# Kernel optimization log

Measured on AMD Instinct MI355X. Metric: run time of the kernel, lower is better.

The kernel has to match this reference:

```python
import jax, jax.numpy as jnp
import numpy as np

IN_FEATURES = 1024
OUT_FEATURES = 1024
BATCH = 32
SEQ = 1024
EPS = 1e-8


def setup_inputs() -> dict:
    key = jax.random.key(0)
    k1, k2, k3 = jax.random.split(key, 3)
    Efou = jax.random.normal(k1, (BATCH, SEQ, IN_FEATURES), dtype=jnp.float32)
    y = jax.random.normal(k2, (BATCH, IN_FEATURES), dtype=jnp.float32)
    weight = jax.random.normal(k3, (IN_FEATURES, OUT_FEATURES), dtype=jnp.float32)
    return {"Efou": Efou, "y": y, "weight": weight}


def reference(Efou, y, weight):
    # scale = 1/sqrt(in_features)
    scale = 1.0 / np.sqrt(np.float32(weight.shape[0]))
    ys = y * scale  # (b, i) == per-sample column scaling of weight
    # Demodulation norm: sum_i (scale*W[i,o]*y[b,i])^2 = (ys^2) @ (W^2)
    d = jax.lax.rsqrt(jnp.einsum('bi,io->bo', ys * ys, weight * weight) + EPS)  # (b, o)
    # Efou @ (scale*W*y*d) == ((Efou*ys) @ W) * d  -- same math, avoids (b,i,o) weight
    out = jnp.einsum('bsi,io->bso', Efou * ys[:, None, :], weight) * d[:, None, :]
    return out
```

## Files before the change

kernel.cpp:

```cpp
#include <hip/hip_runtime.h>

#define AS1 __attribute__((address_space(1)))
#define AS3 __attribute__((address_space(3)))

typedef __bf16 bf16x8 __attribute__((ext_vector_type(8)));
typedef float f32x4 __attribute__((ext_vector_type(4)));
typedef unsigned short ushort8 __attribute__((ext_vector_type(8)));

__device__ __forceinline__ unsigned short f2bf(float f) {
  union { float f; unsigned u; } v; v.f = f;
  unsigned u = v.u;
  unsigned r = (u + 0x7fffu + ((u >> 16) & 1u)) >> 16;
  return (unsigned short)r;
}

__global__ __launch_bounds__(256) void prep_kernel(const float* __restrict__ y,
                                                   const float* __restrict__ W,
                                                   float* __restrict__ partial,
                                                   unsigned short* __restrict__ WT) {
  __shared__ float ysq[32][32];
  const int o = blockIdx.x * 256 + threadIdx.x;
  const int i0 = blockIdx.y * 32;
  for (int e = threadIdx.x; e < 1024; e += 256) {
    int il = e >> 5, b = e & 31;
    float t = y[b * 1024 + i0 + il] * 0.03125f;
    ysq[il][b] = t * t;
  }
  __syncthreads();

  f32x4 acc[8] = {};
  ushort8 wb[4];
#pragma unroll
  for (int il = 0; il < 32; ++il) {
    float w = W[(size_t)(i0 + il) * 1024 + o];
    wb[il >> 3][il & 7] = f2bf(w);
    float w2 = w * w;
#pragma unroll
    for (int b4 = 0; b4 < 8; ++b4) {
      f32x4 q = *(const f32x4*)&ysq[il][b4 * 4];
#pragma unroll
      for (int k = 0; k < 4; ++k) acc[b4][k] = fmaf(q[k], w2, acc[b4][k]);
    }
  }
  unsigned short* wt = WT + (size_t)o * 1024 + i0;
#pragma unroll
  for (int q = 0; q < 4; ++q) *(ushort8*)(wt + q * 8) = wb[q];
  float* p = partial + (size_t)blockIdx.y * 32768 + o;
#pragma unroll
  for (int b4 = 0; b4 < 8; ++b4)
#pragma unroll
    for (int k = 0; k < 4; ++k) p[(b4 * 4 + k) * 1024] = acc[b4][k];
}

__global__ __launch_bounds__(256) void xconv_kernel(const float4* __restrict__ E4,
                                                    const float* __restrict__ y,
                                                    unsigned short* __restrict__ X) {
  const size_t total = (size_t)8388608;
  for (size_t g = (size_t)blockIdx.x * blockDim.x + threadIdx.x; g < total;
       g += (size_t)gridDim.x * blockDim.x) {
    float4 v = E4[g];
    size_t e = g * 4;
    int i = (int)(e & 1023);
    int b = (int)(e >> 20);
    float4 yv = *(const float4*)(y + b * 1024 + i);
    ushort4 o;
    o.x = f2bf(v.x * yv.x * 0.03125f);
    o.y = f2bf(v.y * yv.y * 0.03125f);
    o.z = f2bf(v.z * yv.z * 0.03125f);
    o.w = f2bf(v.w * yv.w * 0.03125f);
    *(ushort4*)(X + e) = o;
  }
}

#define NT 16
#define LDS_TILE 65536

#define BAR __builtin_amdgcn_s_barrier()
#define LGKM0 asm volatile("s_waitcnt lgkmcnt(0)" ::: "memory")
#define VM(n) asm volatile("s_waitcnt vmcnt(" #n ")" ::: "memory")
#define SCHB __builtin_amdgcn_sched_barrier(0)
#define PRIO(x) __builtin_amdgcn_s_setprio(x)

#define STG_A(r, t, dst)                                                     \
  __builtin_amdgcn_global_load_lds(                                          \
      (const AS1 void*)(Xs + (size_t)(r) * 64 * 2048 + (t) * 128),           \
      (AS3 void*)((dst) + (r) * 8192 + sldso), 16, 0, 0)
#define STG_B(r, t, dst)                                                     \
  __builtin_amdgcn_global_load_lds(                                          \
      (const AS1 void*)(Ws + (size_t)(r) * 64 * 2048 + (t) * 128),           \
      (AS3 void*)((dst) + 32768 + (r) * 8192 + sldso), 16, 0, 0)

#define RD_A(mh, mi, kk)                                                     \
  (*(const bf16x8*)(Ab + (wr * 128 + ((mh) * 4 + (mi)) * 16 + l15) * 128 +   \
                    ((((kk) * 64 + lhi * 16)) ^ swz_rd)))
#define RD_B(nh, ni, kk)                                                     \
  (*(const bf16x8*)(Bb + (wc * 64 + ((nh) * 2 + (ni)) * 16 + l15) * 128 +    \
                    ((((kk) * 64 + lhi * 16)) ^ swz_rd)))

#define LD_A(mh)                                                             \
  { _Pragma("unroll") for (int mi = 0; mi < 4; ++mi)                         \
      _Pragma("unroll") for (int kk = 0; kk < 2; ++kk)                       \
        a[mi][kk] = RD_A(mh, mi, kk); }
#define LD_B(nh)                                                             \
  { _Pragma("unroll") for (int ni = 0; ni < 2; ++ni)                         \
      _Pragma("unroll") for (int kk = 0; kk < 2; ++kk)                       \
        bfr[ni][kk] = RD_B(nh, ni, kk); }

#define MM(mh, nh)                                                           \
  do {                                                                       \
    _Pragma("unroll") for (int mi = 0; mi < 4; ++mi)                         \
      _Pragma("unroll") for (int ni = 0; ni < 2; ++ni)                       \
        _Pragma("unroll") for (int kk = 0; kk < 2; ++kk)                     \
          acc[(mh) * 4 + mi][(nh) * 2 + ni] =                                \
              __builtin_amdgcn_mfma_f32_16x16x32_bf16(                       \
                  a[mi][kk], bfr[ni][kk], acc[(mh) * 4 + mi][(nh) * 2 + ni], \
                  0, 0, 0);                                                  \
  } while (0)

__global__ __launch_bounds__(512, 2) void gemm8d_kernel(
    const unsigned short* __restrict__ X, const unsigned short* __restrict__ WT,
    const float* __restrict__ dpart, float* __restrict__ out) {
  extern __shared__ char lds[];
  float* dtab = (float*)(lds + 2 * LDS_TILE);

  const int tid = threadIdx.x;
  const int bid = blockIdx.x;
  const int wg = (bid & 7) * 64 + (bid >> 3);
  const int bm = wg >> 2, bn = wg & 3;
  const int m0 = bm * 256, n0 = bn * 256;
  const int b = m0 >> 10;

  const int w = tid >> 6, l = tid & 63;
  const int wr = w >> 2, wc = w & 3;
  const int l15 = l & 15, lhi = l >> 4;
  const int swz_rd = (l15 & 7) << 4;

  const int srow = tid >> 3;
  const int scb = ((tid & 7) << 4) ^ ((srow & 7) << 4);
  const char* Xs = (const char*)X + (size_t)(m0 + srow) * 2048 + scb;
  const char* Ws = (const char*)WT + (size_t)(n0 + srow) * 2048 + scb;
  const int sldso = tid * 16;

  f32x4 acc[8][4] = {};
  bf16x8 a[4][2], bfr[2][2];

  char* buf0 = lds;
  char* buf1 = lds + LDS_TILE;

  if (tid < 256) {
    const float* dp = dpart + b * 1024 + n0 + tid;
    float s = 0.f;
#pragma unroll 8
    for (int is = 0; is < 32; ++is) s += dp[(size_t)is * 32768];
    dtab[tid] = rsqrtf(s + 1e-8f);
  }
  __syncthreads();

  STG_A(0, 0, buf0); STG_A(2, 0, buf0); STG_A(1, 0, buf0); STG_A(3, 0, buf0);
  STG_B(0, 0, buf0); STG_B(1, 0, buf0); STG_B(2, 0, buf0); STG_B(3, 0, buf0);
  STG_A(0, 1, buf1); STG_A(2, 1, buf1); STG_A(1, 1, buf1); STG_A(3, 1, buf1);
  VM(4);
  BAR;

  for (int t = 0; t < NT - 2; ++t) {
    const char* Ab = lds + (t & 1) * LDS_TILE;
    const char* Bb = Ab + 32768;
    char* dB = lds + ((t + 1) & 1) * LDS_TILE;
    char* dA = lds + (t & 1) * LDS_TILE;
    const int t1 = t + 1, t2 = t + 2;
    LD_A(0); LD_B(0);
    STG_B(0, t1, dB); STG_B(1, t1, dB);
    BAR; LGKM0; SCHB; PRIO(1); MM(0, 0); PRIO(0); SCHB; BAR;
    LD_B(1);
    STG_B(2, t1, dB); STG_B(3, t1, dB);
    BAR; LGKM0; SCHB; PRIO(1); MM(0, 1); PRIO(0); SCHB; BAR;
    LD_A(1); LD_B(0);
    STG_A(0, t2, dA); STG_A(2, t2, dA);
    BAR; LGKM0; SCHB; PRIO(1); MM(1, 0); PRIO(0); SCHB; BAR;
    LD_B(1);
    STG_A(1, t2, dA); STG_A(3, t2, dA);
    BAR; LGKM0; SCHB; PRIO(1); MM(1, 1); PRIO(0); SCHB;
    VM(4);
    BAR;
  }

  {
    const int t = NT - 2;
    const char* Ab = lds + (t & 1) * LDS_TILE;
    const char* Bb = Ab + 32768;
    char* dB = lds + ((t + 1) & 1) * LDS_TILE;
    const int t1 = t + 1;
    LD_A(0); LD_B(0);
    STG_B(0, t1, dB); STG_B(1, t1, dB);
    BAR; LGKM0; SCHB; PRIO(1); MM(0, 0); PRIO(0); SCHB; BAR;
    LD_B(1);
    STG_B(2, t1, dB); STG_B(3, t1, dB);
    BAR; LGKM0; SCHB; PRIO(1); MM(0, 1); PRIO(0); SCHB; BAR;
    LD_A(1); LD_B(0);
    BAR; LGKM0; SCHB; PRIO(1); MM(1, 0); PRIO(0); SCHB; BAR;
    LD_B(1);
    BAR; LGKM0; SCHB; PRIO(1); MM(1, 1); PRIO(0); SCHB;
    VM(0);
    BAR;
  }

  {
    const char* Ab = lds + ((NT - 1) & 1) * LDS_TILE;
    const char* Bb = Ab + 32768;
    LD_A(0); LD_B(0);
    BAR; LGKM0; SCHB; PRIO(1); MM(0, 0); PRIO(0); SCHB; BAR;
    LD_B(1);
    BAR; LGKM0; SCHB; PRIO(1); MM(0, 1); PRIO(0); SCHB; BAR;
    LD_A(1); LD_B(0);
    BAR; LGKM0; SCHB; PRIO(1); MM(1, 0); PRIO(0); SCHB; BAR;
    LD_B(1);
    BAR; LGKM0; SCHB; PRIO(1); MM(1, 1); PRIO(0); SCHB;
  }

  const int lc0 = wc * 64 + l15;
  float dv[4];
#pragma unroll
  for (int nf = 0; nf < 4; ++nf) dv[nf] = dtab[lc0 + nf * 16];
#pragma unroll
  for (int mf = 0; mf < 8; ++mf) {
#pragma unroll
    for (int j = 0; j < 4; ++j) {
      const int row = m0 + wr * 128 + mf * 16 + lhi * 4 + j;
      float* orow = out + (size_t)row * 1024 + n0 + lc0;
#pragma unroll
      for (int nf = 0; nf < 4; ++nf) orow[nf * 16] = acc[mf][nf][j] * dv[nf];
    }
  }
}

extern "C" void kernel_launch(void* const* d_in, const int* in_sizes, int n_in,
                              void* d_out, int out_size, void* d_ws, size_t ws_size,
                              hipStream_t stream) {
  const float* Efou = (const float*)d_in[0];
  const float* y    = (const float*)d_in[1];
  const float* W    = (const float*)d_in[2];
  float* out = (float*)d_out;

  unsigned short* X  = (unsigned short*)d_ws;
  unsigned short* WT = X + (size_t)32768 * 1024;
  float* dpart       = (float*)(WT + (size_t)1024 * 1024);

  hipFuncSetAttribute((const void*)gemm8d_kernel,
                      hipFuncAttributeMaxDynamicSharedMemorySize, 132096);

  prep_kernel<<<dim3(4, 32), 256, 0, stream>>>(y, W, dpart, WT);
  xconv_kernel<<<2048, 256, 0, stream>>>((const float4*)Efou, y, X);
  gemm8d_kernel<<<512, 512, 132096, stream>>>(X, WT, dpart, out);
}
```

Before: 135.1 us.

## Switch GEMM to 32x32x16 MFMA and merge prep kernels into one launch

The GEMM inner loop now uses 32x32x16 bf16 MFMA with matching fragment reads and accumulator layout instead of 16x16x32. This reduces LDS fragment loads per MFMA and instruction count. The weight-prep and Efou-conversion kernels are fused into a single launch split by block index, removing one kernel launch boundary. The epilogue is rewritten for the 32x32 accumulator layout, which changes register pressure and store patterns.

After: 152.6 us. +13.0%, slower.

```diff
diff --git a/kernel.cpp b/kernel.cpp
--- a/kernel.cpp
+++ b/kernel.cpp
@@ -5,6 +5,7 @@
 
 typedef __bf16 bf16x8 __attribute__((ext_vector_type(8)));
 typedef float f32x4 __attribute__((ext_vector_type(4)));
+typedef float f32x16 __attribute__((ext_vector_type(16)));
 typedef unsigned short ushort8 __attribute__((ext_vector_type(8)));
 
 __device__ __forceinline__ unsigned short f2bf(float f) {
@@ -14,61 +15,60 @@
   return (unsigned short)r;
 }
 
-__global__ __launch_bounds__(256) void prep_kernel(const float* __restrict__ y,
-                                                   const float* __restrict__ W,
-                                                   float* __restrict__ partial,
-                                                   unsigned short* __restrict__ WT) {
+__global__ __launch_bounds__(256) void prepx_kernel(
+    const float* __restrict__ y, const float* __restrict__ W,
+    const float4* __restrict__ E4, float* __restrict__ partial,
+    unsigned short* __restrict__ WT, unsigned short* __restrict__ X) {
   __shared__ float ysq[32][32];
-  const int o = blockIdx.x * 256 + threadIdx.x;
-  const int i0 = blockIdx.y * 32;
-  for (int e = threadIdx.x; e < 1024; e += 256) {
-    int il = e >> 5, b = e & 31;
-    float t = y[b * 1024 + i0 + il] * 0.03125f;
-    ysq[il][b] = t * t;
-  }
-  __syncthreads();
-
-  f32x4 acc[8] = {};
-  ushort8 wb[4];
-#pragma unroll
-  for (int il = 0; il < 32; ++il) {
-    float w = W[(size_t)(i0 + il) * 1024 + o];
-    wb[il >> 3][il & 7] = f2bf(w);
-    float w2 = w * w;
-#pragma unroll
-    for (int b4 = 0; b4 < 8; ++b4) {
-      f32x4 q = *(const f32x4*)&ysq[il][b4 * 4];
-#pragma unroll
-      for (int k = 0; k < 4; ++k) acc[b4][k] = fmaf(q[k], w2, acc[b4][k]);
-    }
-  }
-  unsigned short* wt = WT + (size_t)o * 1024 + i0;
-#pragma unroll
-  for (int q = 0; q < 4; ++q) *(ushort8*)(wt + q * 8) = wb[q];
-  float* p = partial + (size_t)blockIdx.y * 32768 + o;
-#pragma unroll
-  for (int b4 = 0; b4 < 8; ++b4)
-#pragma unroll
-    for (int k = 0; k < 4; ++k) p[(b4 * 4 + k) * 1024] = acc[b4][k];
-}
-
-__global__ __launch_bounds__(256) void xconv_kernel(const float4* __restrict__ E4,
-                                                    const float* __restrict__ y,
-                                                    unsigned short* __restrict__ X) {
-  const size_t total = (size_t)8388608;
-  for (size_t g = (size_t)blockIdx.x * blockDim.x + threadIdx.x; g < total;
-       g += (size_t)gridDim.x * blockDim.x) {
-    float4 v = E4[g];
-    size_t e = g * 4;
-    int i = (int)(e & 1023);
-    int b = (int)(e >> 20);
-    float4 yv = *(const float4*)(y + b * 1024 + i);
-    ushort4 o;
-    o.x = f2bf(v.x * yv.x * 0.03125f);
-    o.y = f2bf(v.y * yv.y * 0.03125f);
-    o.z = f2bf(v.z * yv.z * 0.03125f);
-    o.w = f2bf(v.w * yv.w * 0.03125f);
-    *(ushort4*)(X + e) = o;
+  const int bid = blockIdx.x;
+  if (bid < 128) {
+    const int o = (bid & 3) * 256 + threadIdx.x;
+    const int i0 = (bid >> 2) * 32;
+    for (int e = threadIdx.x; e < 1024; e += 256) {
+      int il = e >> 5, b = e & 31;
+      float t = y[b * 1024 + i0 + il] * 0.03125f;
+      ysq[il][b] = t * t;
+    }
+    __syncthreads();
+
+    f32x4 acc[8] = {};
+    ushort8 wb[4];
+#pragma unroll
+    for (int il = 0; il < 32; ++il) {
+      float w = W[(size_t)(i0 + il) * 1024 + o];
+      wb[il >> 3][il & 7] = f2bf(w);
+      float w2 = w * w;
+#pragma unroll
+      for (int b4 = 0; b4 < 8; ++b4) {
+        f32x4 q = *(const f32x4*)&ysq[il][b4 * 4];
+#pragma unroll
+        for (int k = 0; k < 4; ++k) acc[b4][k] = fmaf(q[k], w2, acc[b4][k]);
+      }
+    }
+    unsigned short* wt = WT + (size_t)o * 1024 + i0;
+#pragma unroll
+    for (int q = 0; q < 4; ++q) *(ushort8*)(wt + q * 8) = wb[q];
+    float* p = partial + (size_t)(bid >> 2) * 32768 + o;
+#pragma unroll
+    for (int b4 = 0; b4 < 8; ++b4)
+#pragma unroll
+      for (int k = 0; k < 4; ++k) p[(b4 * 4 + k) * 1024] = acc[b4][k];
+  } else {
+    const size_t total = (size_t)8388608;
+    for (size_t g = (size_t)(bid - 128) * 256 + threadIdx.x; g < total;
+         g += (size_t)2048 * 256) {
+      float4 v = E4[g];
+      size_t e = g * 4;
+      int i = (int)(e & 1023);
+      int b = (int)(e >> 20);
+      float4 yv = *(const float4*)(y + b * 1024 + i);
+      ushort4 o;
+      o.x = f2bf(v.x * yv.x * 0.03125f);
+      o.y = f2bf(v.y * yv.y * 0.03125f);
+      o.z = f2bf(v.z * yv.z * 0.03125f);
+      o.w = f2bf(v.w * yv.w * 0.03125f);
+      *(ushort4*)(X + e) = o;
+    }
   }
 }
 
@@ -90,34 +90,29 @@
       (const AS1 void*)(Ws + (size_t)(r) * 64 * 2048 + (t) * 128),           \
       (AS3 void*)((dst) + 32768 + (r) * 8192 + sldso), 16, 0, 0)
 
-#define RD_A(mh, mi, kk)                                                     \
-  (*(const bf16x8*)(Ab + (wr * 128 + ((mh) * 4 + (mi)) * 16 + l15) * 128 +   \
-                    ((((kk) * 64 + lhi * 16)) ^ swz_rd)))
-#define RD_B(nh, ni, kk)                                                     \
-  (*(const bf16x8*)(Bb + (wc * 64 + ((nh) * 2 + (ni)) * 16 + l15) * 128 +    \
-                    ((((kk) * 64 + lhi * 16)) ^ swz_rd)))
+#define RD_A(mh, mi, ks)                                                     \
+  (*(const bf16x8*)(Ab + (wr * 128 + ((mh) * 2 + (mi)) * 32 + l31) * 128 +   \
+                    ((((ks) * 32 + lq * 16)) ^ swz32)))
+#define RD_B(nh, ks)                                                         \
+  (*(const bf16x8*)(Bb + (wc * 64 + (nh) * 32 + l31) * 128 +                 \
+                    ((((ks) * 32 + lq * 16)) ^ swz32)))
 
 #define LD_A(mh)                                                             \
-  { _Pragma("unroll") for (int mi = 0; mi < 4; ++mi)                         \
-      _Pragma("unroll") for (int kk = 0; kk < 2; ++kk)                       \
-        a[mi][kk] = RD_A(mh, mi, kk); }
+  { _Pragma("unroll") for (int mi = 0; mi < 2; ++mi)                         \
+      _Pragma("unroll") for (int ks = 0; ks < 4; ++ks)                       \
+        a[mi][ks] = RD_A(mh, mi, ks); }
 #define LD_B(nh)                                                             \
-  { _Pragma("unroll") for (int ni = 0; ni < 2; ++ni)                         \
-      _Pragma("unroll") for (int kk = 0; kk < 2; ++kk)                       \
-        bfr[ni][kk] = RD_B(nh, ni, kk); }
+  { _Pragma("unroll") for (int ks = 0; ks < 4; ++ks) bfr[ks] = RD_B(nh, ks); }
 
 #define MM(mh, nh)                                                           \
   do {                                                                       \
-    _Pragma("unroll") for (int mi = 0; mi < 4; ++mi)                         \
-      _Pragma("unroll") for (int ni = 0; ni < 2; ++ni)                       \
-        _Pragma("unroll") for (int kk = 0; kk < 2; ++kk)                     \
-          acc[(mh) * 4 + mi][(nh) * 2 + ni] =                                \
-              __builtin_amdgcn_mfma_f32_16x16x32_bf16(                       \
-                  a[mi][kk], bfr[ni][kk], acc[(mh) * 4 + mi][(nh) * 2 + ni], \
-                  0, 0, 0);                                                  \
+    _Pragma("unroll") for (int mi = 0; mi < 2; ++mi)                         \
+      _Pragma("unroll") for (int ks = 0; ks < 4; ++ks)                       \
+        acc[(mh) * 2 + mi][nh] = __builtin_amdgcn_mfma_f32_32x32x16_bf16(    \
+            a[mi][ks], bfr[ks], acc[(mh) * 2 + mi][nh], 0, 0, 0);            \
   } while (0)
 
-__global__ __launch_bounds__(512, 2) void gemm8d_kernel(
+__global__ __launch_bounds__(512, 2) void gemm32_kernel(
     const unsigned short* __restrict__ X, const unsigned short* __restrict__ WT,
     const float* __restrict__ dpart, float* __restrict__ out) {
   extern __shared__ char lds[];
@@ -132,8 +127,8 @@
 
   const int w = tid >> 6, l = tid & 63;
   const int wr = w >> 2, wc = w & 3;
-  const int l15 = l & 15, lhi = l >> 4;
-  const int swz_rd = (l15 & 7) << 4;
+  const int l31 = l & 31, lq = l >> 5;
+  const int swz32 = (l & 7) << 4;
 
   const int srow = tid >> 3;
   const int scb = ((tid & 7) << 4) ^ ((srow & 7) << 4);
@@ -141,8 +136,8 @@
   const char* Ws = (const char*)WT + (size_t)(n0 + srow) * 2048 + scb;
   const int sldso = tid * 16;
 
-  f32x4 acc[8][4] = {};
-  bf16x8 a[4][2], bfr[2][2];
+  f32x16 acc[4][2] = {};
+  bf16x8 a[2][4], bfr[4];
 
   char* buf0 = lds;
   char* buf1 = lds + LDS_TILE;
@@ -217,18 +212,20 @@
     BAR; LGKM0; SCHB; PRIO(1); MM(1, 1); PRIO(0); SCHB;
   }
 
-  const int lc0 = wc * 64 + l15;
-  float dv[4];
-#pragma unroll
-  for (int nf = 0; nf < 4; ++nf) dv[nf] = dtab[lc0 + nf * 16];
-#pragma unroll
-  for (int mf = 0; mf < 8; ++mf) {
-#pragma unroll
-    for (int j = 0; j < 4; ++j) {
-      const int row = m0 + wr * 128 + mf * 16 + lhi * 4 + j;
-      float* orow = out + (size_t)row * 1024 + n0 + lc0;
-#pragma unroll
-      for (int nf = 0; nf < 4; ++nf) orow[nf * 16] = acc[mf][nf][j] * dv[nf];
+  float dvv[2];
+#pragma unroll
+  for (int nf = 0; nf < 2; ++nf) dvv[nf] = dtab[wc * 64 + nf * 32 + l31];
+#pragma unroll
+  for (int mf = 0; mf < 4; ++mf) {
+#pragma unroll
+    for (int nf = 0; nf < 2; ++nf) {
+      const int col = n0 + wc * 64 + nf * 32 + l31;
+#pragma unroll
+      for (int reg = 0; reg < 16; ++reg) {
+        const int row =
+            m0 + wr * 128 + mf * 32 + (reg & 3) + 8 * (reg >> 2) + 4 * lq;
+        out[(size_t)row * 1024 + col] = acc[mf][nf][reg] * dvv[nf];
+      }
     }
   }
 }
@@ -245,10 +242,9 @@
   unsigned short* WT = X + (size_t)32768 * 1024;
   float* dpart       = (float*)(WT + (size_t)1024 * 1024);
 
-  hipFuncSetAttribute((const void*)gemm8d_kernel,
+  hipFuncSetAttribute((const void*)gemm32_kernel,
                       hipFuncAttributeMaxDynamicSharedMemorySize, 132096);
 
-  prep_kernel<<<dim3(4, 32), 256, 0, stream>>>(y, W, dpart, WT);
-  xconv_kernel<<<2048, 256, 0, stream>>>((const float4*)Efou, y, X);
-  gemm8d_kernel<<<512, 512, 132096, stream>>>(X, WT, dpart, out);
-}
+  prepx_kernel<<<2176, 256, 0, stream>>>(y, W, (const float4*)Efou, dpart, WT, X);
+  gemm32_kernel<<<512, 512, 132096, stream>>>(X, WT, dpart, out);
+}
```

## Merge prep and X-convert kernels; compute demod factors in a separate small kernel

Applied to the files above, without the earlier changes.

Combines the weight-prep and activation-conversion kernels into one launch, with block ranges split by role, so the two run concurrently instead of back to back. The demodulation reduction moves out of the GEMM prologue into a tiny dedicated kernel. This removes the per-block strided partial-sum reads and the extra __syncthreads before the GEMM pipeline starts, and shrinks GEMM LDS slightly. The cost is an extra kernel launch, and the epilogue now reads demod factors from global memory instead of LDS.

Result: slower. 142.7 us (+5.7%).

```diff
diff --git a/kernel.cpp b/kernel.cpp
--- a/kernel.cpp
+++ b/kernel.cpp
@@ -14,62 +14,70 @@
   return (unsigned short)r;
 }
 
-__global__ __launch_bounds__(256) void prep_kernel(const float* __restrict__ y,
-                                                   const float* __restrict__ W,
-                                                   float* __restrict__ partial,
-                                                   unsigned short* __restrict__ WT) {
+__global__ __launch_bounds__(256) void prepx_kernel(
+    const float* __restrict__ y, const float* __restrict__ W,
+    const float4* __restrict__ E4, float* __restrict__ partial,
+    unsigned short* __restrict__ WT, unsigned short* __restrict__ X) {
   __shared__ float ysq[32][32];
-  const int o = blockIdx.x * 256 + threadIdx.x;
-  const int i0 = blockIdx.y * 32;
-  for (int e = threadIdx.x; e < 1024; e += 256) {
-    int il = e >> 5, b = e & 31;
-    float t = y[b * 1024 + i0 + il] * 0.03125f;
-    ysq[il][b] = t * t;
-  }
-  __syncthreads();
-
-  f32x4 acc[8] = {};
-  ushort8 wb[4];
-#pragma unroll
-  for (int il = 0; il < 32; ++il) {
-    float w = W[(size_t)(i0 + il) * 1024 + o];
-    wb[il >> 3][il & 7] = f2bf(w);
-    float w2 = w * w;
-#pragma unroll
-    for (int b4 = 0; b4 < 8; ++b4) {
-      f32x4 q = *(const f32x4*)&ysq[il][b4 * 4];
-#pragma unroll
-      for (int k = 0; k < 4; ++k) acc[b4][k] = fmaf(q[k], w2, acc[b4][k]);
-    }
-  }
-  unsigned short* wt = WT + (size_t)o * 1024 + i0;
-#pragma unroll
-  for (int q = 0; q < 4; ++q) *(ushort8*)(wt + q * 8) = wb[q];
-  float* p = partial + (size_t)blockIdx.y * 32768 + o;
-#pragma unroll
-  for (int b4 = 0; b4 < 8; ++b4)
-#pragma unroll
-    for (int k = 0; k < 4; ++k) p[(b4 * 4 + k) * 1024] = acc[b4][k];
-}
-
-__global__ __launch_bounds__(256) void xconv_kernel(const float4* __restrict__ E4,
-                                                    const float* __restrict__ y,
-                                                    unsigned short* __restrict__ X) {
-  const size_t total = (size_t)8388608;
-  for (size_t g = (size_t)blockIdx.x * blockDim.x + threadIdx.x; g < total;
-       g += (size_t)gridDim.x * blockDim.x) {
-    float4 v = E4[g];
-    size_t e = g * 4;
-    int i = (int)(e & 1023);
-    int b = (int)(e >> 20);
-    float4 yv = *(const float4*)(y + b * 1024 + i);
-    ushort4 o;
-    o.x = f2bf(v.x * yv.x * 0.03125f);
-    o.y = f2bf(v.y * yv.y * 0.03125f);
-    o.z = f2bf(v.z * yv.z * 0.03125f);
-    o.w = f2bf(v.w * yv.w * 0.03125f);
-    *(ushort4*)(X + e) = o;
-  }
+  const int bid = blockIdx.x;
+  if (bid < 128) {
+    const int o = (bid & 3) * 256 + threadIdx.x;
+    const int i0 = (bid >> 2) * 32;
+    for (int e = threadIdx.x; e < 1024; e += 256) {
+      int il = e >> 5, b = e & 31;
+      float t = y[b * 1024 + i0 + il] * 0.03125f;
+      ysq[il][b] = t * t;
+    }
+    __syncthreads();
+
+    f32x4 acc[8] = {};
+    ushort8 wb[4];
+#pragma unroll
+    for (int il = 0; il < 32; ++il) {
+      float w = W[(size_t)(i0 + il) * 1024 + o];
+      wb[il >> 3][il & 7] = f2bf(w);
+      float w2 = w * w;
+#pragma unroll
+      for (int b4 = 0; b4 < 8; ++b4) {
+        f32x4 q = *(const f32x4*)&ysq[il][b4 * 4];
+#pragma unroll
+        for (int k = 0; k < 4; ++k) acc[b4][k] = fmaf(q[k], w2, acc[b4][k]);
+      }
+    }
+    unsigned short* wt = WT + (size_t)o * 1024 + i0;
+#pragma unroll
+    for (int q = 0; q < 4; ++q) *(ushort8*)(wt + q * 8) = wb[q];
+    float* p = partial + (size_t)(bid >> 2) * 32768 + o;
+#pragma unroll
+    for (int b4 = 0; b4 < 8; ++b4)
+#pragma unroll
+      for (int k = 0; k < 4; ++k) p[(b4 * 4 + k) * 1024] = acc[b4][k];
+  } else {
+    const size_t total = (size_t)8388608;
+    for (size_t g = (size_t)(bid - 128) * 256 + threadIdx.x; g < total;
+         g += (size_t)2048 * 256) {
+      float4 v = E4[g];
+      size_t e = g * 4;
+      int i = (int)(e & 1023);
+      int b = (int)(e >> 20);
+      float4 yv = *(const float4*)(y + b * 1024 + i);
+      ushort4 o;
+      o.x = f2bf(v.x * yv.x * 0.03125f);
+      o.y = f2bf(v.y * yv.y * 0.03125f);
+      o.z = f2bf(v.z * yv.z * 0.03125f);
+      o.w = f2bf(v.w * yv.w * 0.03125f);
+      *(ushort4*)(X + e) = o;
+    }
+  }
+}
+
+__global__ __launch_bounds__(256) void dcalc_b_kernel(const float* __restrict__ partial,
+                                                      float* __restrict__ dmod) {
+  const int bo = blockIdx.x * 256 + threadIdx.x;
+  float acc = 0.f;
+#pragma unroll 8
+  for (int is = 0; is < 32; ++is) acc += partial[(size_t)is * 32768 + bo];
+  dmod[bo] = rsqrtf(acc + 1e-8f);
 }
 
 #define NT 16
@@ -119,16 +127,13 @@
 
 __global__ __launch_bounds__(512, 2) void gemm8d_kernel(
     const unsigned short* __restrict__ X, const unsigned short* __restrict__ WT,
-    const float* __restrict__ dpart, float* __restrict__ out) {
+    const float* __restrict__ dmod, float* __restrict__ out) {
   extern __shared__ char lds[];
-  float* dtab = (float*)(lds + 2 * LDS_TILE);
-
   const int tid = threadIdx.x;
   const int bid = blockIdx.x;
   const int wg = (bid & 7) * 64 + (bid >> 3);
   const int bm = wg >> 2, bn = wg & 3;
   const int m0 = bm * 256, n0 = bn * 256;
-  const int b = m0 >> 10;
 
   const int w = tid >> 6, l = tid & 63;
   const int wr = w >> 2, wc = w & 3;
@@ -146,15 +151,6 @@
 
   char* buf0 = lds;
   char* buf1 = lds + LDS_TILE;
-
-  if (tid < 256) {
-    const float* dp = dpart + b * 1024 + n0 + tid;
-    float s = 0.f;
-#pragma unroll 8
-    for (int is = 0; is < 32; ++is) s += dp[(size_t)is * 32768];
-    dtab[tid] = rsqrtf(s + 1e-8f);
-  }
-  __syncthreads();
 
   STG_A(0, 0, buf0); STG_A(2, 0, buf0); STG_A(1, 0, buf0); STG_A(3, 0, buf0);
   STG_B(0, 0, buf0); STG_B(1, 0, buf0); STG_B(2, 0, buf0); STG_B(3, 0, buf0);
@@ -217,16 +213,17 @@
     BAR; LGKM0; SCHB; PRIO(1); MM(1, 1); PRIO(0); SCHB;
   }
 
-  const int lc0 = wc * 64 + l15;
+  const int b = m0 >> 10;
+  const int col0 = n0 + wc * 64 + l15;
   float dv[4];
 #pragma unroll
-  for (int nf = 0; nf < 4; ++nf) dv[nf] = dtab[lc0 + nf * 16];
+  for (int nf = 0; nf < 4; ++nf) dv[nf] = dmod[b * 1024 + col0 + nf * 16];
 #pragma unroll
   for (int mf = 0; mf < 8; ++mf) {
 #pragma unroll
     for (int j = 0; j < 4; ++j) {
       const int row = m0 + wr * 128 + mf * 16 + lhi * 4 + j;
-      float* orow = out + (size_t)row * 1024 + n0 + lc0;
+      float* orow = out + (size_t)row * 1024 + col0;
 #pragma unroll
       for (int nf = 0; nf < 4; ++nf) orow[nf * 16] = acc[mf][nf][j] * dv[nf];
     }
@@ -244,11 +241,12 @@
   unsigned short* X  = (unsigned short*)d_ws;
   unsigned short* WT = X + (size_t)32768 * 1024;
   float* dpart       = (float*)(WT + (size_t)1024 * 1024);
+  float* dmod        = dpart + (size_t)32 * 32768;
 
   hipFuncSetAttribute((const void*)gemm8d_kernel,
-                      hipFuncAttributeMaxDynamicSharedMemorySize, 132096);
-
-  prep_kernel<<<dim3(4, 32), 256, 0, stream>>>(y, W, dpart, WT);
-  xconv_kernel<<<2048, 256, 0, stream>>>((const float4*)Efou, y, X);
-  gemm8d_kernel<<<512, 512, 132096, stream>>>(X, WT, dpart, out);
-}
+                      hipFuncAttributeMaxDynamicSharedMemorySize, 131072);
+
+  prepx_kernel<<<2176, 256, 0, stream>>>(y, W, (const float4*)Efou, dpart, WT, X);
+  dcalc_b_kernel<<<128, 256, 0, stream>>>(dpart, dmod);
+  gemm8d_kernel<<<512, 512, 131072, stream>>>(X, WT, dmod, out);
+}
```
